# Kernel tuning notes

Measured on AMD Instinct MI355X. Metric: run time of the kernel, lower is better.

## Reference

```python
import jax, jax.numpy as jnp
import numpy as np

B, S, D, H = 8, 1024, 512, 8
Dh = D // H
MASK_FILL = -1e32


def _xavier_uniform(key, shape):
    fan_in, fan_out = shape[-1], shape[-2] if len(shape) > 1 else shape[-1]
    limit = float(np.sqrt(6.0 / (fan_in + fan_out)))
    return jax.random.uniform(key, shape, jnp.float32, -limit, limit)


def setup_inputs() -> dict:
    key = jax.random.key(0)
    ks = jax.random.split(key, 8)
    q = jax.random.normal(ks[0], (B, S, D), jnp.float32)
    k = jax.random.normal(ks[1], (B, S, D), jnp.float32)
    v = jax.random.normal(ks[2], (B, S, D), jnp.float32)
    # causal mask, broadcast over batch and heads
    mask = jnp.tril(jnp.ones((S, S), dtype=bool))[None, None]
    # key_query_same=True -> one shared W for q and k
    Wq = _xavier_uniform(ks[3], (D, D)); bq = jnp.zeros((D,), jnp.float32)
    Wv = _xavier_uniform(ks[4], (D, D)); bv = jnp.zeros((D,), jnp.float32)
    Wo = _xavier_uniform(ks[5], (D, D)); bo = jnp.zeros((D,), jnp.float32)
    # gammas: (H,1,1), xavier_uniform with fan_in=fan_out=1 -> limit sqrt(3)
    lim = float(np.sqrt(3.0))
    gammas = jax.random.uniform(ks[6], (H, 1, 1), jnp.float32, -lim, lim)
    return {"q": q, "k": k, "v": v, "mask": mask,
            "Wq": Wq, "bq": bq, "Wv": Wv, "bv": bv,
            "Wo": Wo, "bo": bo, "gammas": gammas}


def reference(q, k, v, mask, Wq, bq, Wv, bv, Wo, bo, gammas):
    b, s, d = q.shape
    # projections (key_query_same -> Wq used for both q and k)
    qh = (jnp.einsum("bsd,ed->bse", q, Wq) + bq).reshape(b, s, H, Dh).transpose(0, 2, 1, 3)
    kh = (jnp.einsum("bsd,ed->bse", k, Wq) + bq).reshape(b, s, H, Dh).transpose(0, 2, 1, 3)
    vh = (jnp.einsum("bsd,ed->bse", v, Wv) + bv).reshape(b, s, H, Dh).transpose(0, 2, 1, 3)

    scale = 1.0 / jnp.sqrt(jnp.asarray(Dh, jnp.float32))
    scores = jnp.einsum("bhqd,bhkd->bhqk", qh, kh) * scale  # [B,H,S,S]

    # --- distance-decay effect (no-grad in original) ---
    pos = jnp.arange(s, dtype=jnp.float32)
    position_effect = jnp.abs(pos[None, :] - pos[:, None])[None, None]  # [1,1,S,S]
    scores_ = jax.nn.softmax(jnp.where(mask, scores, MASK_FILL), axis=-1)
    distcum = jnp.cumsum(scores_, axis=-1)
    disttotal = jnp.sum(scores_, axis=-1, keepdims=True)
    dist_scores = jnp.sqrt(jnp.clip((disttotal - distcum) * position_effect, 0.0, None))
    dist_scores = jax.lax.stop_gradient(dist_scores)

    gamma = -jnp.abs(gammas)[None]  # [1,H,1,1]
    total_effect = jnp.clip(jnp.exp(dist_scores * gamma), 1e-5, 1e5)
    scores = scores * total_effect

    scores = jax.nn.softmax(jnp.where(mask, scores, MASK_FILL), axis=-1)
    scores = jnp.where(mask, scores, 0.0)  # hard zero, avoid leakage

    v_ = jnp.einsum("bhqk,bhkd->bhqd", scores, vh)
    concat = v_.transpose(0, 2, 1, 3).reshape(b, s, d)
    output = jnp.einsum("bsd,ed->bse", concat, Wo) + bo
    return output, scores
```

## Files before the change

kernel.cpp:

```cpp
#include <hip/hip_runtime.h>
#include <hip/hip_bf16.h>

#define PB 8
#define PS 1024
#define PD 512
#define PH 8

typedef __attribute__((ext_vector_type(8))) short short8;
typedef __attribute__((ext_vector_type(4))) float f32x4;

__device__ inline ushort f2bf(float x) {
    union { float f; unsigned u; } c; c.f = x;
    unsigned u = c.u + 0x7fffu + ((c.u >> 16) & 1u);
    return (ushort)(u >> 16);
}
__device__ inline float bf2f(ushort u) {
    union { unsigned u; float f; } c; c.u = (unsigned)u << 16; return c.f;
}

__device__ inline void gload16(const void* g, void* l) {
    __builtin_amdgcn_global_load_lds(
        (const __attribute__((address_space(1))) void*)g,
        (__attribute__((address_space(3))) void*)l, 16, 0, 0);
}

__global__ __launch_bounds__(256)
void cast_all(const float* __restrict__ q, const float* __restrict__ k,
              const float* __restrict__ v, const float* __restrict__ Wq,
              const float* __restrict__ Wv, const float* __restrict__ Wo,
              ushort* __restrict__ q_bf, ushort* __restrict__ k_bf,
              ushort* __restrict__ v_bf, ushort* __restrict__ Wq_bf,
              ushort* __restrict__ Wv_bf, ushort* __restrict__ Wo_bf)
{
    const int bid = blockIdx.x;
    const float* s; ushort* d; int base;
    if      (bid < 4096)  { s = q;  d = q_bf;  base = bid; }
    else if (bid < 8192)  { s = k;  d = k_bf;  base = bid - 4096; }
    else if (bid < 12288) { s = v;  d = v_bf;  base = bid - 8192; }
    else if (bid < 12544) { s = Wq; d = Wq_bf; base = bid - 12288; }
    else if (bid < 12800) { s = Wv; d = Wv_bf; base = bid - 12544; }
    else                  { s = Wo; d = Wo_bf; base = bid - 12800; }
    const int i = base * 256 + threadIdx.x;
    const float4 x = ((const float4*)s)[i];
    ushort4 o;
    o.x = f2bf(x.x); o.y = f2bf(x.y); o.z = f2bf(x.z); o.w = f2bf(x.w);
    ((ushort4*)d)[i] = o;
}

__global__ __launch_bounds__(256)
void proj3(const ushort* __restrict__ q_bf, const ushort* __restrict__ k_bf,
           const ushort* __restrict__ v_bf, const ushort* __restrict__ Wq_bf,
           const ushort* __restrict__ Wv_bf, const float* __restrict__ bq,
           const float* __restrict__ bv, ushort* __restrict__ qh,
           ushort* __restrict__ kh, ushort* __restrict__ vhT)
{
    const int z = blockIdx.z;
    const ushort* A = (z == 0) ? q_bf : (z == 1) ? k_bf : v_bf;
    const ushort* B = (z == 2) ? Wv_bf : Wq_bf;
    const float* bias = (z == 2) ? bv : bq;

    __shared__ __align__(16) ushort As[128 * 64];
    __shared__ __align__(16) ushort Bs[128 * 64];
    const int tid = threadIdx.x;
    const int lane = tid & 63;
    const int wave = tid >> 6;
    const int wr = wave >> 1, wc = wave & 1;
    const int bm = blockIdx.x * 128, bn = blockIdx.y * 128;
    const int lrow = lane >> 3;
    const int lcol = (lane & 7) * 8;

    f32x4 acc[4][4] = {};

    for (int k0 = 0; k0 < 512; k0 += 64) {
#pragma unroll
        for (int i = 0; i < 4; ++i) {
            const int c = wave * 4 + i;
            gload16(A + (size_t)(bm + c * 8 + lrow) * 512 + k0 + lcol, &As[c * 512]);
            gload16(B + (size_t)(bn + c * 8 + lrow) * 512 + k0 + lcol, &Bs[c * 512]);
        }
        __syncthreads();
        short8 af[2][4], bf[2][4];
#pragma unroll
        for (int kk = 0; kk < 2; ++kk) {
#pragma unroll
            for (int m = 0; m < 4; ++m)
                af[kk][m] = *(const short8*)&As[(wr * 64 + m * 16 + (lane & 15)) * 64 + kk * 32 + (lane >> 4) * 8];
#pragma unroll
            for (int n = 0; n < 4; ++n)
                bf[kk][n] = *(const short8*)&Bs[(wc * 64 + n * 16 + (lane & 15)) * 64 + kk * 32 + (lane >> 4) * 8];
        }
#pragma unroll
        for (int kk = 0; kk < 2; ++kk)
#pragma unroll
            for (int m = 0; m < 4; ++m)
#pragma unroll
                for (int n = 0; n < 4; ++n)
                    acc[m][n] = __builtin_amdgcn_mfma_f32_16x16x32_bf16(af[kk][m], bf[kk][n], acc[m][n], 0, 0, 0);
        __syncthreads();
    }

#pragma unroll
    for (int m = 0; m < 4; ++m)
#pragma unroll
        for (int n = 0; n < 4; ++n) {
            const int row0 = bm + wr * 64 + m * 16 + (lane >> 4) * 4;
            const int col  = bn + wc * 64 + n * 16 + (lane & 15);
            const int b = row0 >> 10, s0 = row0 & 1023;
            const int h = col >> 6, d = col & 63;
            if (z == 2) {
                ushort4 o;
                o.x = f2bf(acc[m][n][0] + bias[col]);
                o.y = f2bf(acc[m][n][1] + bias[col]);
                o.z = f2bf(acc[m][n][2] + bias[col]);
                o.w = f2bf(acc[m][n][3] + bias[col]);
                *(ushort4*)&vhT[((size_t)((b * 8 + h) * 64 + d)) * 1024 + s0] = o;
            } else {
                ushort* out = z ? kh : qh;
#pragma unroll
                for (int r = 0; r < 4; ++r)
                    out[(((size_t)(b * 8 + h)) * 1024 + s0 + r) * 64 + d] =
                        f2bf(acc[m][n][r] + bias[col]);
            }
        }
}

__global__ __launch_bounds__(256)
void qk_mfma(const ushort* __restrict__ qh, const ushort* __restrict__ kh,
             float* __restrict__ scores)
{
    const int d0 = blockIdx.x;
    const int bh = d0 & 63;
    const int pair = d0 >> 6;
    const int kb = pair & 7, qb = pair >> 3;
    const int tid = threadIdx.x;
    if (kb > qb) {
        float* S = scores + ((size_t)bh << 20);
        const f32x4 z = {};
#pragma unroll
        for (int it = 0; it < 16; ++it) {
            const int f = it * 256 + tid;
            const int row = f >> 5, c4 = f & 31;
            __builtin_nontemporal_store(z,
                (f32x4*)&S[(size_t)(qb * 128 + row) * 1024 + kb * 128 + c4 * 4]);
        }
        return;
    }
    __shared__ __align__(16) ushort As[128 * 64];
    __shared__ __align__(16) ushort Bs[128 * 64];
    const int lane = tid & 63, wave = tid >> 6;
    const int wr = wave >> 1, wc = wave & 1;
    const ushort* Ab = qh + ((size_t)bh * PS + qb * 128) * 64;
    const ushort* Bb = kh + ((size_t)bh * PS + kb * 128) * 64;

#pragma unroll
    for (int i = 0; i < 4; ++i) {
        const int c = wave * 4 + i;
        gload16(Ab + c * 512 + lane * 8, &As[c * 512]);
        gload16(Bb + c * 512 + lane * 8, &Bs[c * 512]);
    }
    __syncthreads();

    f32x4 acc[4][4] = {};
    short8 af[2][4], bf[2][4];
#pragma unroll
    for (int kk = 0; kk < 2; ++kk) {
#pragma unroll
        for (int m = 0; m < 4; ++m)
            af[kk][m] = *(const short8*)&As[(wr * 64 + m * 16 + (lane & 15)) * 64 + kk * 32 + (lane >> 4) * 8];
#pragma unroll
        for (int n = 0; n < 4; ++n)
            bf[kk][n] = *(const short8*)&Bs[(wc * 64 + n * 16 + (lane & 15)) * 64 + kk * 32 + (lane >> 4) * 8];
    }
#pragma unroll
    for (int kk = 0; kk < 2; ++kk)
#pragma unroll
        for (int m = 0; m < 4; ++m)
#pragma unroll
            for (int n = 0; n < 4; ++n)
                acc[m][n] = __builtin_amdgcn_mfma_f32_16x16x32_bf16(af[kk][m], bf[kk][n], acc[m][n], 0, 0, 0);

    ushort* Sr = (ushort*)(scores + ((size_t)bh << 20));
#pragma unroll
    for (int m = 0; m < 4; ++m)
#pragma unroll
        for (int n = 0; n < 4; ++n)
#pragma unroll
            for (int r = 0; r < 4; ++r) {
                const int row = qb * 128 + wr * 64 + m * 16 + (lane >> 4) * 4 + r;
                const int col = kb * 128 + wc * 64 + n * 16 + (lane & 15);
                Sr[(size_t)row * 2048 + col] = f2bf(acc[m][n][r] * 0.125f);
            }
}

__global__ __launch_bounds__(1024)
void rowpv2(float* __restrict__ scores, const ushort* __restrict__ vhT,
            const float* __restrict__ gammas, ushort* __restrict__ attn)
{
    const int d0 = blockIdx.x;
    const int bh = d0 & 63, h = bh & 7;
    const int b = bh >> 3;
    const int rb = d0 >> 6;
    const int w = threadIdx.x >> 6;
    const int lane = threadIdx.x & 63;
    const int i = rb * 16 + w;
    const int nt = (rb >> 2) + 1;
    const int G = (rb >> 4) + 1;
    const int base = lane * 4 * G;
    const int lim = ((i >> 7) + 1) * 128;

    __shared__ __align__(16) ushort P[16 * 1024];
    __shared__ float RED[4][16][68];

    float* srow = scores + ((size_t)bh << 20) + ((size_t)i << 10);
    const ushort* rraw = (const ushort*)srow;

    union U4 { uint2 v; ushort u[4]; };
    float l[16];
#pragma unroll
    for (int g = 0; g < 4; ++g) {
        if (g < G) {
            U4 a; a.v = *(const uint2*)(rraw + base + g * 4);
#pragma unroll
            for (int j = 0; j < 4; ++j)
                l[g * 4 + j] = (base + g * 4 + j <= i) ? bf2f(a.u[j]) : -3.0e38f;
        }
    }

    float m1 = -3.0e38f;
#pragma unroll
    for (int g = 0; g < 4; ++g) if (g < G)
#pragma unroll
        for (int j = 0; j < 4; ++j) m1 = fmaxf(m1, l[g * 4 + j]);
#pragma unroll
    for (int off = 32; off; off >>= 1) m1 = fmaxf(m1, __shfl_xor(m1, off));

    float cum[16];
    float lsum = 0.f;
#pragma unroll
    for (int g = 0; g < 4; ++g) if (g < G)
#pragma unroll
        for (int j = 0; j < 4; ++j) {
            const int c = g * 4 + j;
            const float e = (base + c <= i) ? __expf(l[c] - m1) : 0.f;
            lsum += e;
            cum[c] = lsum;
        }
    float incl = lsum;
#pragma unroll
    for (int off = 1; off < 64; off <<= 1) {
        const float y = __shfl_up(incl, off);
        if (lane >= off) incl += y;
    }
    const float excl = incl - lsum;
    const float es = __shfl(incl, 63);
    const float inv_es = __builtin_amdgcn_rcpf(es);
    const float gamma = -fabsf(gammas[h]);

    float m2 = -3.0e38f;
#pragma unroll
    for (int g = 0; g < 4; ++g) if (g < G)
#pragma unroll
        for (int j = 0; j < 4; ++j) {
            const int c = g * 4 + j;
            if (base + c <= i) {
                const float pe = (float)(i - (base + c));
                const float sfx = fmaxf((es - (excl + cum[c])) * inv_es, 0.f);
                const float dist = __builtin_amdgcn_sqrtf(sfx * pe);
                const float eff = fmaxf(__expf(gamma * dist), 1e-5f);
                l[c] *= eff;
                m2 = fmaxf(m2, l[c]);
            }
        }
#pragma unroll
    for (int off = 32; off; off >>= 1) m2 = fmaxf(m2, __shfl_xor(m2, off));

    float s2 = 0.f;
#pragma unroll
    for (int g = 0; g < 4; ++g) if (g < G)
#pragma unroll
        for (int j = 0; j < 4; ++j) {
            const int c = g * 4 + j;
            const float p = (base + c <= i) ? __expf(l[c] - m2) : 0.f;
            l[c] = p; s2 += p;
        }
#pragma unroll
    for (int off = 32; off; off >>= 1) s2 += __shfl_xor(s2, off);
    const float inv2 = __builtin_amdgcn_rcpf(s2);
#pragma unroll
    for (int g = 0; g < 4; ++g) if (g < G)
#pragma unroll
        for (int j = 0; j < 4; ++j) l[g * 4 + j] *= inv2;

#pragma unroll
    for (int g = 0; g < 4; ++g) {
        if (g < G) {
            U4 p;
#pragma unroll
            for (int j = 0; j < 4; ++j) p.u[j] = f2bf(l[g * 4 + j]);
            const int col = base + g * 4;
            const int lc = col >> 3;
            const int sp = (lc & ~7) | ((lc ^ w) & 7);
            *(uint2*)&P[w * 1024 + sp * 8 + (col & 7)] = p.v;
        }
    }
    __syncthreads();

#pragma unroll
    for (int g = 0; g < 4; ++g) {
        if (g < G && base + g * 4 < lim) {
            f32x4 v;
            v[0] = l[g * 4 + 0]; v[1] = l[g * 4 + 1];
            v[2] = l[g * 4 + 2]; v[3] = l[g * 4 + 3];
            __builtin_nontemporal_store(v, (f32x4*)&srow[base + g * 4]);
        }
    }

    const int kq = w >> 2, nn = w & 3;
    const int row16 = lane & 15, kg = lane >> 4;
    const ushort* vb = vhT + ((size_t)bh << 16) + (size_t)(nn * 16 + row16) * 1024;
    f32x4 acc = {};
    for (int t = kq; t < nt; t += 4) {
#pragma unroll
        for (int kk = 0; kk < 2; ++kk) {
            const int chunk = t * 8 + ((kk * 4 + kg) ^ (row16 & 7));
            const short8 af = *(const short8*)&P[row16 * 1024 + chunk * 8];
            const short8 bf = *(const short8*)&vb[t * 64 + kk * 32 + kg * 8];
            acc = __builtin_amdgcn_mfma_f32_16x16x32_bf16(af, bf, acc, 0, 0, 0);
        }
    }

#pragma unroll
    for (int r = 0; r < 4; ++r)
        RED[kq][kg * 4 + r][nn * 16 + row16] = acc[r];
    __syncthreads();
    const float o = RED[0][w][lane] + RED[1][w][lane] +
                    RED[2][w][lane] + RED[3][w][lane];
    attn[((size_t)(b * 1024 + i)) * 512 + h * 64 + lane] = f2bf(o);
}

__global__ __launch_bounds__(256)
void gemm_out(const ushort* __restrict__ A, const ushort* __restrict__ B,
              const float* __restrict__ bias, float* __restrict__ out)
{
    __shared__ __align__(16) ushort As[128 * 64];
    __shared__ __align__(16) ushort Bs[128 * 64];
    const int tid = threadIdx.x;
    const int lane = tid & 63;
    const int wave = tid >> 6;
    const int wr = wave >> 1, wc = wave & 1;
    const int bm = blockIdx.x * 128, bn = blockIdx.y * 128;
    const int lrow = lane >> 3;
    const int lcol = (lane & 7) * 8;

    f32x4 acc[4][4] = {};

    for (int k0 = 0; k0 < 512; k0 += 64) {
#pragma unroll
        for (int i = 0; i < 4; ++i) {
            const int c = wave * 4 + i;
            gload16(A + (size_t)(bm + c * 8 + lrow) * 512 + k0 + lcol, &As[c * 512]);
            gload16(B + (size_t)(bn + c * 8 + lrow) * 512 + k0 + lcol, &Bs[c * 512]);
        }
        __syncthreads();
        short8 af[2][4], bf[2][4];
#pragma unroll
        for (int kk = 0; kk < 2; ++kk) {
#pragma unroll
            for (int m = 0; m < 4; ++m)
                af[kk][m] = *(const short8*)&As[(wr * 64 + m * 16 + (lane & 15)) * 64 + kk * 32 + (lane >> 4) * 8];
#pragma unroll
            for (int n = 0; n < 4; ++n)
                bf[kk][n] = *(const short8*)&Bs[(wc * 64 + n * 16 + (lane & 15)) * 64 + kk * 32 + (lane >> 4) * 8];
        }
#pragma unroll
        for (int kk = 0; kk < 2; ++kk)
#pragma unroll
            for (int m = 0; m < 4; ++m)
#pragma unroll
                for (int n = 0; n < 4; ++n)
                    acc[m][n] = __builtin_amdgcn_mfma_f32_16x16x32_bf16(af[kk][m], bf[kk][n], acc[m][n], 0, 0, 0);
        __syncthreads();
    }

#pragma unroll
    for (int m = 0; m < 4; ++m)
#pragma unroll
        for (int n = 0; n < 4; ++n)
#pragma unroll
            for (int r = 0; r < 4; ++r) {
                const int row = bm + wr * 64 + m * 16 + (lane >> 4) * 4 + r;
                const int col = bn + wc * 64 + n * 16 + (lane & 15);
                out[(size_t)row * 512 + col] = acc[m][n][r] + bias[col];
            }
}

extern "C" void kernel_launch(void* const* d_in, const int* in_sizes, int n_in,
                              void* d_out, int out_size, void* d_ws, size_t ws_size,
                              hipStream_t stream)
{
    const float* q      = (const float*)d_in[0];
    const float* k      = (const float*)d_in[1];
    const float* v      = (const float*)d_in[2];
    const float* Wq     = (const float*)d_in[4];
    const float* bq     = (const float*)d_in[5];
    const float* Wv     = (const float*)d_in[6];
    const float* bv     = (const float*)d_in[7];
    const float* Wo     = (const float*)d_in[8];
    const float* bo     = (const float*)d_in[9];
    const float* gammas = (const float*)d_in[10];

    float* out    = (float*)d_out;
    float* scores = out + (size_t)PB * PS * PD;

    char* w = (char*)d_ws;
    ushort* q_bf  = (ushort*)(w);
    ushort* k_bf  = (ushort*)(w + (8u  << 20));
    ushort* v_bf  = (ushort*)(w + (16u << 20));
    ushort* Wq_bf = (ushort*)(w + (24u << 20));
    ushort* Wv_bf = (ushort*)(w + (24u << 20) + (1u << 19));
    ushort* Wo_bf = (ushort*)(w + (25u << 20));
    ushort* qh    = (ushort*)(w + (26u << 20));
    ushort* kh    = (ushort*)(w + (34u << 20));
    ushort* vhT   = (ushort*)(w + (42u << 20));
    ushort* attn  = (ushort*)(w + (50u << 20));

    cast_all<<<13056, 256, 0, stream>>>(q, k, v, Wq, Wv, Wo,
                                        q_bf, k_bf, v_bf, Wq_bf, Wv_bf, Wo_bf);

    proj3<<<dim3(64, 4, 3), 256, 0, stream>>>(q_bf, k_bf, v_bf, Wq_bf, Wv_bf,
                                              bq, bv, qh, kh, vhT);

    qk_mfma<<<4096, 256, 0, stream>>>(qh, kh, scores);
    rowpv2<<<4096, 1024, 0, stream>>>(scores, vhT, gammas, attn);

    gemm_out<<<dim3(64, 4), 256, 0, stream>>>(attn, Wo_bf, bo, out);
}
```

Baseline: 241.7 us.

## Split row kernel into 8-row blocks and fuse second softmax max pass

Rows-per-block drops from 16 to 8 with 512-thread blocks and doubled grid, and the PV MFMA tiles reuse 8 rows with duplicated lanes discarded. The per-element cumulative array and second max reduction are replaced by a running prefix and a static upper bound max(m1,0) for the second softmax, computing exp directly in one pass. This aims to cut registers, LDS and a cross-lane reduction to improve occupancy, at the cost of half-wasted MFMA work and a looser softmax stabilizer.

```diff
diff --git a/kernel.cpp b/kernel.cpp
--- a/kernel.cpp
+++ b/kernel.cpp
@@ -192,8 +192,8 @@
             }
 }
 
-__global__ __launch_bounds__(1024)
-void rowpv2(float* __restrict__ scores, const ushort* __restrict__ vhT,
+__global__ __launch_bounds__(512, 8)
+void rowpv3(float* __restrict__ scores, const ushort* __restrict__ vhT,
             const float* __restrict__ gammas, ushort* __restrict__ attn)
 {
     const int d0 = blockIdx.x;
@@ -202,14 +202,14 @@
     const int rb = d0 >> 6;
     const int w = threadIdx.x >> 6;
     const int lane = threadIdx.x & 63;
-    const int i = rb * 16 + w;
-    const int nt = (rb >> 2) + 1;
-    const int G = (rb >> 4) + 1;
+    const int i = rb * 8 + w;
+    const int nt = (rb >> 3) + 1;
+    const int G = (nt + 3) >> 2;
     const int base = lane * 4 * G;
     const int lim = ((i >> 7) + 1) * 128;
 
-    __shared__ __align__(16) ushort P[16 * 1024];
-    __shared__ float RED[4][16][68];
+    __shared__ __align__(16) ushort P[8 * 1024];
+    __shared__ float RED[2][8][68];
 
     float* srow = scores + ((size_t)bh << 20) + ((size_t)i << 10);
     const ushort* rraw = (const ushort*)srow;
@@ -234,17 +234,11 @@
 #pragma unroll
     for (int off = 32; off; off >>= 1) m1 = fmaxf(m1, __shfl_xor(m1, off));
 
-    float cum[16];
     float lsum = 0.f;
 #pragma unroll
     for (int g = 0; g < 4; ++g) if (g < G)
 #pragma unroll
-        for (int j = 0; j < 4; ++j) {
-            const int c = g * 4 + j;
-            const float e = (base + c <= i) ? __expf(l[c] - m1) : 0.f;
-            lsum += e;
-            cum[c] = lsum;
-        }
+        for (int j = 0; j < 4; ++j) lsum += __expf(l[g * 4 + j] - m1);
     float incl = lsum;
 #pragma unroll
     for (int off = 1; off < 64; off <<= 1) {
@@ -255,33 +249,26 @@
     const float es = __shfl(incl, 63);
     const float inv_es = __builtin_amdgcn_rcpf(es);
     const float gamma = -fabsf(gammas[h]);
-
-    float m2 = -3.0e38f;
+    const float M2 = fmaxf(m1, 0.f);
+
+    float racc = excl;
+    float s2 = 0.f;
 #pragma unroll
     for (int g = 0; g < 4; ++g) if (g < G)
 #pragma unroll
         for (int j = 0; j < 4; ++j) {
             const int c = g * 4 + j;
             if (base + c <= i) {
+                racc += __expf(l[c] - m1);
+                const float sfxn = fmaxf((es - racc) * inv_es, 0.f);
                 const float pe = (float)(i - (base + c));
-                const float sfx = fmaxf((es - (excl + cum[c])) * inv_es, 0.f);
-                const float dist = __builtin_amdgcn_sqrtf(sfx * pe);
+                const float dist = __builtin_amdgcn_sqrtf(sfxn * pe);
                 const float eff = fmaxf(__expf(gamma * dist), 1e-5f);
-                l[c] *= eff;
-                m2 = fmaxf(m2, l[c]);
+                const float p = __expf(l[c] * eff - M2);
+                l[c] = p; s2 += p;
+            } else {
+                l[c] = 0.f;
             }
-        }
-#pragma unroll
-    for (int off = 32; off; off >>= 1) m2 = fmaxf(m2, __shfl_xor(m2, off));
-
-    float s2 = 0.f;
-#pragma unroll
-    for (int g = 0; g < 4; ++g) if (g < G)
-#pragma unroll
-        for (int j = 0; j < 4; ++j) {
-            const int c = g * 4 + j;
-            const float p = (base + c <= i) ? __expf(l[c] - m2) : 0.f;
-            l[c] = p; s2 += p;
         }
 #pragma unroll
     for (int off = 32; off; off >>= 1) s2 += __shfl_xor(s2, off);
@@ -317,24 +304,26 @@
 
     const int kq = w >> 2, nn = w & 3;
     const int row16 = lane & 15, kg = lane >> 4;
+    const int arow = lane & 7;
     const ushort* vb = vhT + ((size_t)bh << 16) + (size_t)(nn * 16 + row16) * 1024;
     f32x4 acc = {};
-    for (int t = kq; t < nt; t += 4) {
+    for (int t = kq; t < nt; t += 2) {
 #pragma unroll
         for (int kk = 0; kk < 2; ++kk) {
-            const int chunk = t * 8 + ((kk * 4 + kg) ^ (row16 & 7));
-            const short8 af = *(const short8*)&P[row16 * 1024 + chunk * 8];
+            const int chunk = t * 8 + ((kk * 4 + kg) ^ arow);
+            const short8 af = *(const short8*)&P[arow * 1024 + chunk * 8];
             const short8 bf = *(const short8*)&vb[t * 64 + kk * 32 + kg * 8];
             acc = __builtin_amdgcn_mfma_f32_16x16x32_bf16(af, bf, acc, 0, 0, 0);
         }
     }
 
-#pragma unroll
-    for (int r = 0; r < 4; ++r)
-        RED[kq][kg * 4 + r][nn * 16 + row16] = acc[r];
+    if (kg < 2) {
+#pragma unroll
+        for (int r = 0; r < 4; ++r)
+            RED[kq][kg * 4 + r][nn * 16 + row16] = acc[r];
+    }
     __syncthreads();
-    const float o = RED[0][w][lane] + RED[1][w][lane] +
-                    RED[2][w][lane] + RED[3][w][lane];
+    const float o = RED[0][w][lane] + RED[1][w][lane];
     attn[((size_t)(b * 1024 + i)) * 512 + h * 64 + lane] = f2bf(o);
 }
 
@@ -431,7 +420,7 @@
                                               bq, bv, qh, kh, vhT);
 
     qk_mfma<<<4096, 256, 0, stream>>>(qh, kh, scores);
-    rowpv2<<<4096, 1024, 0, stream>>>(scores, vhT, gammas, attn);
+    rowpv3<<<8192, 512, 0, stream>>>(scores, vhT, gammas, attn);
 
     gemm_out<<<dim3(64, 4), 256, 0, stream>>>(attn, Wo_bf, bo, out);
 }
```

Result: no change. 238.1 us (-1.5%).
